# Kernel optimization log

Measured on AMD Instinct MI355X. Metric: run time of the kernel, lower is better.

The kernel has to match this reference:

```python
import jax, jax.numpy as jnp
import numpy as np

V = 32000   # target_vocab_size
E = 512     # embedding_dim
L = 2       # enc_lstm_layers
HD = 512    # enc_lstm_hidden_dim (bidirectional encoder)
H = 2 * HD  # decoder LSTM hidden size
B = 16
T = 128
BOS = 1
CTX = L * 2 * HD          # stepwise context dim = 2048
IN0 = E + CTX             # decoder LSTM layer-0 input dim = 2560


def setup_inputs() -> dict:
    key = jax.random.key(0)
    ks = jax.random.split(key, 12)
    def w(k, shape, fan_in):
        return jax.random.normal(k, shape, jnp.float32) * np.float32(1.0 / np.sqrt(fan_in))
    return {
        "enc_lstm_hidden": jax.random.normal(ks[0], (2 * L, B, HD), jnp.float32),
        "enc_lstm_ctxt": jax.random.normal(ks[1], (2 * L, B, HD), jnp.float32),
        "minibatch_target": jax.random.randint(ks[2], (B, T), 0, V, dtype=jnp.int32),
        "emb": w(ks[3], (V, E), E),
        "w_ih_0": w(ks[4], (4 * H, IN0), IN0),
        "w_hh_0": w(ks[5], (4 * H, H), H),
        "b_ih_0": jnp.zeros((4 * H,), jnp.float32),
        "b_hh_0": jnp.zeros((4 * H,), jnp.float32),
        "w_ih_1": w(ks[6], (4 * H, H), H),
        "w_hh_1": w(ks[7], (4 * H, H), H),
        "b_ih_1": jnp.zeros((4 * H,), jnp.float32),
        "b_hh_1": jnp.zeros((4 * H,), jnp.float32),
        "fc_w": w(ks[8], (V, H), H),
        "fc_b": jnp.zeros((V,), jnp.float32),
    }


def _lstm_layer(x_seq, h0, c0, w_ih, w_hh, b):
    """x_seq: [T, B, in]; returns top outputs [T, B, H]. torch gate order i,f,g,o."""
    def step(carry, x):
        h, c = carry
        g = x @ w_ih.T + h @ w_hh.T + b
        i, f, gg, o = jnp.split(g, 4, axis=-1)
        c = jax.nn.sigmoid(f) * c + jax.nn.sigmoid(i) * jnp.tanh(gg)
        h = jax.nn.sigmoid(o) * jnp.tanh(c)
        return (h, c), h
    (hT, cT), ys = jax.lax.scan(step, (h0, c0), x_seq)
    return ys, hT, cT


def reference(enc_lstm_hidden, enc_lstm_ctxt, minibatch_target, emb,
              w_ih_0, w_hh_0, b_ih_0, b_hh_0,
              w_ih_1, w_hh_1, b_ih_1, b_hh_1, fc_w, fc_b):
    # _reshape_encoder_state: [2L,B,HD] -> [L,B,2HD] (interleave fwd/bwd per layer)
    def reshape_state(s):
        return s.reshape(L, 2, B, HD).transpose(0, 2, 1, 3).reshape(L, B, 2 * HD)
    h0 = reshape_state(enc_lstm_hidden)
    c0 = reshape_state(enc_lstm_ctxt)
    # stepwise input context: [B, 2L*HD]
    ctx = jnp.transpose(enc_lstm_hidden, (1, 0, 2)).reshape(B, CTX)
    # teacher forcing: prev tokens = [BOS, target[:, :-1]]
    tokens = jnp.concatenate(
        [jnp.full((B, 1), BOS, minibatch_target.dtype), minibatch_target[:, :-1]], axis=1)
    tok_emb = emb[tokens]                                   # [B,T,E]
    ctx_b = jnp.broadcast_to(ctx[:, None, :], (B, T, CTX))  # [B,T,CTX]
    x = jnp.concatenate([tok_emb, ctx_b], axis=-1).transpose(1, 0, 2)  # [T,B,IN0]
    x, _, _ = _lstm_layer(x, h0[0], c0[0], w_ih_0, w_hh_0, b_ih_0 + b_hh_0)
    x, _, _ = _lstm_layer(x, h0[1], c0[1], w_ih_1, w_hh_1, b_ih_1 + b_hh_1)
    out = jnp.tanh(x)                                       # [T,B,H]
    logits = jnp.einsum('tbh,vh->btv', out, fc_w) + fc_b    # [B,T,V]
    return logits
```

## Files before the change

kernel.cpp:

```cpp
#include <hip/hip_runtime.h>


#define NBLK 256

typedef float f32x4 __attribute__((ext_vector_type(4)));
typedef __bf16 bf16x8 __attribute__((ext_vector_type(8)));
typedef unsigned short u16;

__device__ __forceinline__ float sigf(float x) { return 1.0f / (1.0f + __expf(-x)); }
__device__ __forceinline__ float tanh_(float x) {
  x = fminf(15.0f, fmaxf(-15.0f, x));
  float e = __expf(2.0f * x);
  return (e - 1.0f) / (e + 1.0f);
}

__device__ __forceinline__ u16 f2bf(float f) {
  __bf16 h = (__bf16)f;
  return __builtin_bit_cast(u16, h);
}

__device__ __forceinline__ void st_cv16(u16* p, u16 v) {
  unsigned vv = v;
  asm volatile("global_store_short %0, %1, off sc0 sc1" :: "v"(p), "v"(vv) : "memory");
}

__device__ __forceinline__ void flag_store(unsigned* p, unsigned v) {
  asm volatile(
      "s_waitcnt vmcnt(0)\n\t"
      "global_store_dword %0, %1, off sc0 sc1"
      :: "v"(p), "v"(v) : "memory");
}

__device__ __forceinline__ void ld4_flags(const unsigned* p, unsigned& a, unsigned& b,
                                          unsigned& c, unsigned& d) {
  asm volatile(
      "global_load_dword %0, %4, off sc0 sc1\n\t"
      "global_load_dword %1, %5, off sc0 sc1\n\t"
      "global_load_dword %2, %6, off sc0 sc1\n\t"
      "global_load_dword %3, %7, off sc0 sc1\n\t"
      "s_waitcnt vmcnt(0)"
      : "=&v"(a), "=&v"(b), "=&v"(c), "=&v"(d)
      : "v"(p), "v"(p + 16), "v"(p + 32), "v"(p + 48)
      : "memory");
}

__device__ __forceinline__ void gsyncf(unsigned step, unsigned* bar) {
  __syncthreads();
  const int tid = threadIdx.x;
  if (tid == 0) flag_store(bar + 16 + blockIdx.x * 16, step);
  if (tid < 64) {
    const unsigned* base = bar + 16 + tid * 64;
    for (;;) {
      unsigned a, b, c, d;
      ld4_flags(base, a, b, c, d);
      bool mine = (a >= step) & (b >= step) & (c >= step) & (d >= step);
      if (__all(mine)) break;
      __builtin_amdgcn_s_sleep(1);
    }
    asm volatile("" ::: "memory");
  }
  __syncthreads();
}

__device__ __forceinline__ void dot4(float& a, float4 wv, float4 xv) {
  a = fmaf(wv.x, xv.x, a);
  a = fmaf(wv.y, xv.y, a);
  a = fmaf(wv.z, xv.z, a);
  a = fmaf(wv.w, xv.w, a);
}

#define MFMA16(ACC, XB, WM, WOFF)                                           \
  _Pragma("unroll")                                                         \
  for (int mm = 0; mm < 16; ++mm) {                                         \
    bf16x8 av = *(const bf16x8*)&XB[fr][mm * 32 + ks8];                     \
    bf16x8 bv = *(const bf16x8*)&WM[fr][(WOFF) + mm * 32 + ks8];            \
    ACC = __builtin_amdgcn_mfma_f32_16x16x32_bf16(av, bv, ACC, 0, 0, 0);    \
  }

__global__ void prep_emb(const int* __restrict__ tgt, const float* __restrict__ emb,
                         u16* __restrict__ x0b) {
  const int g = blockIdx.x * blockDim.x + threadIdx.x;
  const int col8 = (g & 63) * 8;
  const int tb = g >> 6;
  const int t = tb >> 4, b = tb & 15;
  const int tok = (t == 0) ? 1 : tgt[b * 128 + (t - 1)];
  const float* s = emb + (size_t)tok * 512 + col8;
  float4 a = *(const float4*)s;
  float4 bb = *(const float4*)(s + 4);
  __align__(16) u16 r[8] = {f2bf(a.x), f2bf(a.y), f2bf(a.z), f2bf(a.w),
                            f2bf(bb.x), f2bf(bb.y), f2bf(bb.z), f2bf(bb.w)};
  *(uint4*)(x0b + (size_t)tb * 512 + col8) = *(uint4*)r;
}

__global__ __launch_bounds__(256, 1) void prep_ctx(const float* __restrict__ enc_h,
                                                   const float* __restrict__ wih0,
                                                   float* __restrict__ cp) {
  __shared__ float ctx[16][2052];
  const int tid = threadIdx.x;
#pragma unroll
  for (int c = 0; c < 32; ++c) {
    int f4 = tid + c * 256;
    int b = f4 >> 9, kq = f4 & 511;
    *(float4*)&ctx[b][kq * 4] =
        *(const float4*)(enc_h + (kq >> 7) * 8192 + b * 512 + (kq & 127) * 4);
  }
  __syncthreads();
  const int jr = tid >> 4, b = tid & 15;
  const int j = blockIdx.x * 16 + jr;
  const float* w = wih0 + (size_t)j * 2560 + 512;
  float a0 = 0.f, a1 = 0.f, a2 = 0.f, a3 = 0.f;
  for (int k = 0; k < 2048; k += 16) {
    float4 w0 = *(const float4*)(w + k);
    float4 w1 = *(const float4*)(w + k + 4);
    float4 w2 = *(const float4*)(w + k + 8);
    float4 w3 = *(const float4*)(w + k + 12);
    float4 x0 = *(const float4*)&ctx[b][k];
    float4 x1 = *(const float4*)&ctx[b][k + 4];
    float4 x2 = *(const float4*)&ctx[b][k + 8];
    float4 x3 = *(const float4*)&ctx[b][k + 12];
    dot4(a0, w0, x0); dot4(a1, w1, x1); dot4(a2, w2, x2); dot4(a3, w3, x3);
  }
  cp[(size_t)j * 16 + b] = a0 + a1 + a2 + a3;
}

__global__ __launch_bounds__(512, 1) void dec_seq_mf(
    const float* __restrict__ enc_h, const float* __restrict__ enc_c,
    const float* __restrict__ wih0, const float* __restrict__ whh0,
    const float* __restrict__ wih1, const float* __restrict__ whh1,
    const float* __restrict__ bih0, const float* __restrict__ bhh0,
    const float* __restrict__ bih1, const float* __restrict__ bhh1,
    const float* __restrict__ cp, const u16* __restrict__ x0b,
    u16* __restrict__ xr, u16* __restrict__ h1r,
    u16* __restrict__ out2b, unsigned* bar) {
  __shared__ u16 Wa[16][1544];
  __shared__ u16 Wb[16][2056];
  __shared__ u16 xc[2][16][520];
  __shared__ float glsA[16][17];
  __shared__ float glsB[16][17];

  const int tid = threadIdx.x;
  const int wgid = blockIdx.x;
  const int w4 = wgid * 4;
  const int lane = tid & 63;
  const int wave = tid >> 6;
  const int fr = lane & 15;
  const int ks8 = (lane >> 4) * 8;
  unsigned step = 0;

  {
    const int row = tid >> 5;
    const int j = (row >> 2) * 1024 + w4 + (row & 3);
    {
      const int c = (tid & 31) * 16;
      const float* s = wih0 + (size_t)j * 2560 + c;
      __align__(16) u16 r[16];
#pragma unroll
      for (int q = 0; q < 4; ++q) {
        float4 v = *(const float4*)(s + q * 4);
        r[q * 4 + 0] = f2bf(v.x); r[q * 4 + 1] = f2bf(v.y);
        r[q * 4 + 2] = f2bf(v.z); r[q * 4 + 3] = f2bf(v.w);
      }
      *(uint4*)&Wa[row][c] = *(uint4*)&r[0];
      *(uint4*)&Wa[row][c + 8] = *(uint4*)&r[8];
    }
    {
      const int c = (tid & 31) * 32;
      const float* s = whh0 + (size_t)j * 1024 + c;
      __align__(16) u16 r[32];
#pragma unroll
      for (int q = 0; q < 8; ++q) {
        float4 v = *(const float4*)(s + q * 4);
        r[q * 4 + 0] = f2bf(v.x); r[q * 4 + 1] = f2bf(v.y);
        r[q * 4 + 2] = f2bf(v.z); r[q * 4 + 3] = f2bf(v.w);
      }
#pragma unroll
      for (int q = 0; q < 4; ++q) *(uint4*)&Wa[row][512 + c + q * 8] = *(uint4*)&r[q * 8];
    }
    {
      const int c = (tid & 31) * 32;
      const float* s = wih1 + (size_t)j * 1024 + c;
      __align__(16) u16 r[32];
#pragma unroll
      for (int q = 0; q < 8; ++q) {
        float4 v = *(const float4*)(s + q * 4);
        r[q * 4 + 0] = f2bf(v.x); r[q * 4 + 1] = f2bf(v.y);
        r[q * 4 + 2] = f2bf(v.z); r[q * 4 + 3] = f2bf(v.w);
      }
#pragma unroll
      for (int q = 0; q < 4; ++q) *(uint4*)&Wb[row][c + q * 8] = *(uint4*)&r[q * 8];
    }
    {
      const int c = (tid & 31) * 32;
      const float* s = whh1 + (size_t)j * 1024 + c;
      __align__(16) u16 r[32];
#pragma unroll
      for (int q = 0; q < 8; ++q) {
        float4 v = *(const float4*)(s + q * 4);
        r[q * 4 + 0] = f2bf(v.x); r[q * 4 + 1] = f2bf(v.y);
        r[q * 4 + 2] = f2bf(v.z); r[q * 4 + 3] = f2bf(v.w);
      }
#pragma unroll
      for (int q = 0; q < 4; ++q) *(uint4*)&Wb[row][1024 + c + q * 8] = *(uint4*)&r[q * 8];
    }
  }

  const int gdj = tid >> 4;
  const int gb = tid & 15;
  float cpA0 = 0.f, cpA1 = 0.f, cpA2 = 0.f, cpA3 = 0.f;
  float cpB0 = 0.f, cpB1 = 0.f, cpB2 = 0.f, cpB3 = 0.f;
  float c0r = 0.f, c1r = 0.f;
  if (tid < 64) {
    const int jp = w4 + gdj;
    cpA0 = cp[(size_t)(jp) * 16 + gb] + bih0[jp] + bhh0[jp];
    cpA1 = cp[(size_t)(1024 + jp) * 16 + gb] + bih0[1024 + jp] + bhh0[1024 + jp];
    cpA2 = cp[(size_t)(2048 + jp) * 16 + gb] + bih0[2048 + jp] + bhh0[2048 + jp];
    cpA3 = cp[(size_t)(3072 + jp) * 16 + gb] + bih0[3072 + jp] + bhh0[3072 + jp];
    cpB0 = bih1[jp] + bhh1[jp];
    cpB1 = bih1[1024 + jp] + bhh1[1024 + jp];
    cpB2 = bih1[2048 + jp] + bhh1[2048 + jp];
    cpB3 = bih1[3072 + jp] + bhh1[3072 + jp];
    const int dir = jp >> 9, e = jp & 511;
    c0r = enc_c[dir * 8192 + gb * 512 + e];
    c1r = enc_c[(2 + dir) * 8192 + gb * 512 + e];
    st_cv16(xr + gb * 1024 + jp, f2bf(enc_h[dir * 8192 + gb * 512 + e]));
    st_cv16(h1r + gb * 1024 + jp, f2bf(enc_h[(2 + dir) * 8192 + gb * 512 + e]));
  }
  gsyncf(++step, bar);

  const int srow = tid >> 5;
  const int scol = (tid & 31) * 16;

  for (int s = 0; s < 129; ++s) {
    uint4 rA0a = {}, rA0b = {}, rB2a = {}, rB2b = {}, rB3a = {}, rB3b = {};
    uint4 rA1a, rA1b, rA2a, rA2b;
    {
      const u16* slotS = xr + (size_t)s * 16384 + srow * 1024;
      rA1a = *(const uint4*)(slotS + scol);
      rA1b = *(const uint4*)(slotS + scol + 8);
      rA2a = *(const uint4*)(slotS + 512 + scol);
      rA2b = *(const uint4*)(slotS + 512 + scol + 8);
      if (s < 128) {
        const u16* sE = x0b + (size_t)s * 8192 + srow * 512;
        rA0a = *(const uint4*)(sE + scol);
        rA0b = *(const uint4*)(sE + scol + 8);
      }
      if (s >= 1) {
        const u16* sH = h1r + (size_t)(s - 1) * 16384 + srow * 1024;
        rB2a = *(const uint4*)(sH + scol);
        rB2b = *(const uint4*)(sH + scol + 8);
        rB3a = *(const uint4*)(sH + 512 + scol);
        rB3b = *(const uint4*)(sH + 512 + scol + 8);
      }
    }
    f32x4 accA = {0.f, 0.f, 0.f, 0.f}, accB = {0.f, 0.f, 0.f, 0.f};

    if (s < 128) {
      *(uint4*)&xc[0][srow][scol] = rA0a;
      *(uint4*)&xc[0][srow][scol + 8] = rA0b;
    }
    __syncthreads();
    *(uint4*)&xc[1][srow][scol] = rA1a;
    *(uint4*)&xc[1][srow][scol + 8] = rA1b;
    if (wave == 0 && s < 128) { MFMA16(accA, xc[0], Wa, 0) }
    __syncthreads();
    *(uint4*)&xc[0][srow][scol] = rA2a;
    *(uint4*)&xc[0][srow][scol + 8] = rA2b;
    if (wave == 0 && s < 128) { MFMA16(accA, xc[1], Wa, 512) }
    if (wave == 1 && s >= 1) { MFMA16(accB, xc[1], Wb, 0) }
    __syncthreads();
    if (s >= 1) {
      *(uint4*)&xc[1][srow][scol] = rB2a;
      *(uint4*)&xc[1][srow][scol + 8] = rB2b;
    }
    if (wave == 0 && s < 128) { MFMA16(accA, xc[0], Wa, 1024) }
    if (wave == 1 && s >= 1) { MFMA16(accB, xc[0], Wb, 512) }
    __syncthreads();
    if (s >= 1) {
      *(uint4*)&xc[0][srow][scol] = rB3a;
      *(uint4*)&xc[0][srow][scol + 8] = rB3b;
    }
    if (wave == 1 && s >= 1) { MFMA16(accB, xc[1], Wb, 1024) }
    __syncthreads();
    if (wave == 1 && s >= 1) { MFMA16(accB, xc[0], Wb, 1536) }
    if (wave == 0 && s < 128) {
#pragma unroll
      for (int r = 0; r < 4; ++r) glsA[fr][(lane >> 4) * 4 + r] = accA[r];
    }
    if (wave == 1 && s >= 1) {
#pragma unroll
      for (int r = 0; r < 4; ++r) glsB[fr][(lane >> 4) * 4 + r] = accB[r];
    }
    __syncthreads();
    if (tid < 64) {
      const int jp = w4 + gdj;
      if (s < 128) {
        float gi = glsA[gdj][gb] + cpA0;
        float gf = glsA[4 + gdj][gb] + cpA1;
        float gg = glsA[8 + gdj][gb] + cpA2;
        float go = glsA[12 + gdj][gb] + cpA3;
        c0r = sigf(gf) * c0r + sigf(gi) * tanh_(gg);
        float h = sigf(go) * tanh_(c0r);
        st_cv16(xr + (size_t)(s + 1) * 16384 + gb * 1024 + jp, f2bf(h));
      }
      if (s >= 1) {
        float gi = glsB[gdj][gb] + cpB0;
        float gf = glsB[4 + gdj][gb] + cpB1;
        float gg = glsB[8 + gdj][gb] + cpB2;
        float go = glsB[12 + gdj][gb] + cpB3;
        c1r = sigf(gf) * c1r + sigf(gi) * tanh_(gg);
        float h = sigf(go) * tanh_(c1r);
        st_cv16(h1r + (size_t)s * 16384 + gb * 1024 + jp, f2bf(h));
        out2b[((s - 1) * 16 + gb) * 1024 + jp] = f2bf(tanh_(h));
      }
    }
    gsyncf(++step, bar);
  }
}

__global__ __launch_bounds__(256, 2) void fc_gemm_mfma(
    const u16* __restrict__ A, const float* __restrict__ Bw,
    const float* __restrict__ bias, float* __restrict__ C) {
  __shared__ __align__(16) u16 Al[128][40];
  __shared__ __align__(16) u16 Bl[128][40];

  const int tid = threadIdx.x;
  const int m0 = blockIdx.x * 128;
  const int n0 = blockIdx.y * 128;
  const int wave = tid >> 6;
  const int lane = tid & 63;
  const int wm = (wave & 1) * 64;
  const int wn = (wave >> 1) * 64;
  const int fr = lane & 15;
  const int ks = lane >> 4;

  const int srow = tid >> 1;
  const int sh16 = (tid & 1) * 16;

  const u16* Ag = A + (size_t)(m0 + srow) * 1024 + sh16;
  const float* Bg = Bw + (size_t)(n0 + srow) * 1024 + sh16;

  f32x4 acc[4][4] = {};

  for (int k0 = 0; k0 < 1024; k0 += 32) {
    uint4 a0 = *(const uint4*)(Ag + k0);
    uint4 a1 = *(const uint4*)(Ag + k0 + 8);
    float bfv[16];
    *(float4*)&bfv[0] = *(const float4*)(Bg + k0);
    *(float4*)&bfv[4] = *(const float4*)(Bg + k0 + 4);
    *(float4*)&bfv[8] = *(const float4*)(Bg + k0 + 8);
    *(float4*)&bfv[12] = *(const float4*)(Bg + k0 + 12);
    u16 bu[16];
#pragma unroll
    for (int u = 0; u < 16; ++u) bu[u] = f2bf(bfv[u]);

    __syncthreads();
    *(uint4*)&Al[srow][sh16] = a0;
    *(uint4*)&Al[srow][sh16 + 8] = a1;
    *(uint4*)&Bl[srow][sh16] = *(uint4*)&bu[0];
    *(uint4*)&Bl[srow][sh16 + 8] = *(uint4*)&bu[8];
    __syncthreads();

    bf16x8 af[4], bf[4];
#pragma unroll
    for (int i = 0; i < 4; ++i) af[i] = *(const bf16x8*)&Al[wm + i * 16 + fr][ks * 8];
#pragma unroll
    for (int j = 0; j < 4; ++j) bf[j] = *(const bf16x8*)&Bl[wn + j * 16 + fr][ks * 8];
#pragma unroll
    for (int i = 0; i < 4; ++i)
#pragma unroll
      for (int j = 0; j < 4; ++j)
        acc[i][j] = __builtin_amdgcn_mfma_f32_16x16x32_bf16(af[i], bf[j], acc[i][j], 0, 0, 0);
  }

  float bj[4];
#pragma unroll
  for (int j = 0; j < 4; ++j) bj[j] = bias[n0 + wn + j * 16 + fr];

  const int mrb = (lane >> 4) * 4;
#pragma unroll
  for (int i = 0; i < 4; ++i) {
#pragma unroll
    for (int r = 0; r < 4; ++r) {
      const int m = m0 + wm + i * 16 + mrb + r;
      float* dst = C + ((size_t)(m & 15) * 128 + (m >> 4)) * 32000;
#pragma unroll
      for (int j = 0; j < 4; ++j) {
        dst[n0 + wn + j * 16 + fr] = acc[i][j][r] + bj[j];
      }
    }
  }
}

extern "C" void kernel_launch(void* const* d_in, const int* in_sizes, int n_in,
                              void* d_out, int out_size, void* d_ws, size_t ws_size,
                              hipStream_t stream) {
  const float* enc_h = (const float*)d_in[0];
  const float* enc_c = (const float*)d_in[1];
  const int* tgt = (const int*)d_in[2];
  const float* emb = (const float*)d_in[3];
  const float* wih0 = (const float*)d_in[4];
  const float* whh0 = (const float*)d_in[5];
  const float* bih0 = (const float*)d_in[6];
  const float* bhh0 = (const float*)d_in[7];
  const float* wih1 = (const float*)d_in[8];
  const float* whh1 = (const float*)d_in[9];
  const float* bih1 = (const float*)d_in[10];
  const float* bhh1 = (const float*)d_in[11];
  const float* fcw = (const float*)d_in[12];
  const float* fcb = (const float*)d_in[13];
  float* logits = (float*)d_out;

  unsigned* bar = (unsigned*)d_ws;
  hipMemsetAsync(d_ws, 0, 64 + 256 * 64, stream);

  float* cp = (float*)((char*)d_ws + 32768);
  u16* x0b = (u16*)(cp + 65536);
  u16* xr = x0b + 1048576;
  u16* h1r = xr + 2113536;
  u16* out2b = h1r + 2113536;

  prep_emb<<<512, 256, 0, stream>>>(tgt, emb, x0b);
  prep_ctx<<<256, 256, 0, stream>>>(enc_h, wih0, cp);
  dec_seq_mf<<<NBLK, 512, 0, stream>>>(enc_h, enc_c, wih0, whh0, wih1, whh1,
                                       bih0, bhh0, bih1, bhh1, cp, x0b,
                                       xr, h1r, out2b, bar);
  fc_gemm_mfma<<<dim3(16, 250), 256, 0, stream>>>(out2b, fcw, fcb, logits);
}
```

Baseline: 1.098 ms.

## Precompute embedding input projection and split recurrent MFMA work across six waves

The embedding part of the layer-0 input projection is taken out of the sequential loop and computed for all timesteps by a separate bf16 MFMA GEMM (pe_gemm), whose results are added during the gate update. Inside the persistent recurrent kernel, the dot products that used to run serially on waves 0 and 1 are now spread over six waves, one 512-wide K chunk each, with partial sums reduced through shared memory. Each step now needs one barrier to stage inputs instead of several, and one wave keeps part of its weights in registers. The cost is an extra kernel launch, a large fp32 intermediate buffer, and a per-step gather of those values.

```diff
diff --git a/kernel.cpp b/kernel.cpp
--- a/kernel.cpp
+++ b/kernel.cpp
@@ -17,6 +17,13 @@
 __device__ __forceinline__ u16 f2bf(float f) {
   __bf16 h = (__bf16)f;
   return __builtin_bit_cast(u16, h);
+}
+
+__device__ __forceinline__ bf16x8 cvt8(float4 a, float4 b) {
+  bf16x8 v;
+  v[0] = (__bf16)a.x; v[1] = (__bf16)a.y; v[2] = (__bf16)a.z; v[3] = (__bf16)a.w;
+  v[4] = (__bf16)b.x; v[5] = (__bf16)b.y; v[6] = (__bf16)b.z; v[7] = (__bf16)b.w;
+  return v;
 }
 
 __device__ __forceinline__ void st_cv16(u16* p, u16 v) {
@@ -68,14 +75,6 @@
   a = fmaf(wv.z, xv.z, a);
   a = fmaf(wv.w, xv.w, a);
 }
-
-#define MFMA16(ACC, XB, WM, WOFF)                                           \
-  _Pragma("unroll")                                                         \
-  for (int mm = 0; mm < 16; ++mm) {                                         \
-    bf16x8 av = *(const bf16x8*)&XB[fr][mm * 32 + ks8];                     \
-    bf16x8 bv = *(const bf16x8*)&WM[fr][(WOFF) + mm * 32 + ks8];            \
-    ACC = __builtin_amdgcn_mfma_f32_16x16x32_bf16(av, bv, ACC, 0, 0, 0);    \
-  }
 
 __global__ void prep_emb(const int* __restrict__ tgt, const float* __restrict__ emb,
                          u16* __restrict__ x0b) {
@@ -123,84 +122,124 @@
   cp[(size_t)j * 16 + b] = a0 + a1 + a2 + a3;
 }
 
-__global__ __launch_bounds__(512, 1) void dec_seq_mf(
+__global__ __launch_bounds__(256, 2) void pe_gemm(
+    const u16* __restrict__ A, const float* __restrict__ Bw, float* __restrict__ C) {
+  __shared__ __align__(16) u16 Al[128][40];
+  __shared__ __align__(16) u16 Bl[128][40];
+  const int tid = threadIdx.x;
+  const int m0 = blockIdx.x * 128;
+  const int n0 = blockIdx.y * 128;
+  const int wave = tid >> 6;
+  const int lane = tid & 63;
+  const int wm = (wave & 1) * 64;
+  const int wn = (wave >> 1) * 64;
+  const int fr = lane & 15;
+  const int ks = lane >> 4;
+  const int srow = tid >> 1;
+  const int sh16 = (tid & 1) * 16;
+  const u16* Ag = A + (size_t)(m0 + srow) * 512 + sh16;
+  const float* Bg = Bw + (size_t)(n0 + srow) * 2560 + sh16;
+  f32x4 acc[4][4] = {};
+  for (int k0 = 0; k0 < 512; k0 += 32) {
+    uint4 a0 = *(const uint4*)(Ag + k0);
+    uint4 a1 = *(const uint4*)(Ag + k0 + 8);
+    float bfv[16];
+    *(float4*)&bfv[0] = *(const float4*)(Bg + k0);
+    *(float4*)&bfv[4] = *(const float4*)(Bg + k0 + 4);
+    *(float4*)&bfv[8] = *(const float4*)(Bg + k0 + 8);
+    *(float4*)&bfv[12] = *(const float4*)(Bg + k0 + 12);
+    u16 bu[16];
+#pragma unroll
+    for (int u = 0; u < 16; ++u) bu[u] = f2bf(bfv[u]);
+    __syncthreads();
+    *(uint4*)&Al[srow][sh16] = a0;
+    *(uint4*)&Al[srow][sh16 + 8] = a1;
+    *(uint4*)&Bl[srow][sh16] = *(uint4*)&bu[0];
+    *(uint4*)&Bl[srow][sh16 + 8] = *(uint4*)&bu[8];
+    __syncthreads();
+    bf16x8 af[4], bf[4];
+#pragma unroll
+    for (int i = 0; i < 4; ++i) af[i] = *(const bf16x8*)&Al[wm + i * 16 + fr][ks * 8];
+#pragma unroll
+    for (int j = 0; j < 4; ++j) bf[j] = *(const bf16x8*)&Bl[wn + j * 16 + fr][ks * 8];
+#pragma unroll
+    for (int i = 0; i < 4; ++i)
+#pragma unroll
+      for (int j = 0; j < 4; ++j)
+        acc[i][j] = __builtin_amdgcn_mfma_f32_16x16x32_bf16(af[i], bf[j], acc[i][j], 0, 0, 0);
+  }
+  const int mrb = (lane >> 4) * 4;
+#pragma unroll
+  for (int i = 0; i < 4; ++i) {
+#pragma unroll
+    for (int r = 0; r < 4; ++r) {
+      const int m = m0 + wm + i * 16 + mrb + r;
+      float* dst = C + (size_t)m * 4096;
+#pragma unroll
+      for (int j = 0; j < 4; ++j) dst[n0 + wn + j * 16 + fr] = acc[i][j][r];
+    }
+  }
+}
+
+#define BURST_L(ACC, XB, XOFF, WF0)                                        \
+  _Pragma("unroll")                                                        \
+  for (int mm = 0; mm < 16; ++mm) {                                        \
+    bf16x8 av = *(const bf16x8*)&XB[(XOFF) + mm * 520 + lane8];            \
+    bf16x8 bv = *(const bf16x8*)&wf[((WF0) + mm) * 512 + lane8];           \
+    ACC = __builtin_amdgcn_mfma_f32_16x16x32_bf16(av, bv, ACC, 0, 0, 0);   \
+  }
+#define BURST_R(ACC, XB, XOFF)                                             \
+  _Pragma("unroll")                                                        \
+  for (int mm = 0; mm < 16; ++mm) {                                        \
+    bf16x8 av = *(const bf16x8*)&XB[(XOFF) + mm * 520 + lane8];            \
+    ACC = __builtin_amdgcn_mfma_f32_16x16x32_bf16(av, bw[mm], ACC, 0, 0, 0); \
+  }
+
+__global__ __launch_bounds__(512, 1) void dec_seq_mf2(
     const float* __restrict__ enc_h, const float* __restrict__ enc_c,
-    const float* __restrict__ wih0, const float* __restrict__ whh0,
-    const float* __restrict__ wih1, const float* __restrict__ whh1,
+    const float* __restrict__ whh0, const float* __restrict__ wih1,
+    const float* __restrict__ whh1,
     const float* __restrict__ bih0, const float* __restrict__ bhh0,
     const float* __restrict__ bih1, const float* __restrict__ bhh1,
-    const float* __restrict__ cp, const u16* __restrict__ x0b,
+    const float* __restrict__ cp, const float* __restrict__ pe,
     u16* __restrict__ xr, u16* __restrict__ h1r,
     u16* __restrict__ out2b, unsigned* bar) {
-  __shared__ u16 Wa[16][1544];
-  __shared__ u16 Wb[16][2056];
-  __shared__ u16 xc[2][16][520];
-  __shared__ float glsA[16][17];
-  __shared__ float glsB[16][17];
+  __shared__ u16 xf[16640];
+  __shared__ u16 h1f[16640];
+  __shared__ u16 wf[40960];
+  __shared__ float gls[6][16][17];
 
   const int tid = threadIdx.x;
   const int wgid = blockIdx.x;
   const int w4 = wgid * 4;
   const int lane = tid & 63;
   const int wave = tid >> 6;
-  const int fr = lane & 15;
-  const int ks8 = (lane >> 4) * 8;
+  const int lane8 = lane * 8;
   unsigned step = 0;
 
-  {
-    const int row = tid >> 5;
-    const int j = (row >> 2) * 1024 + w4 + (row & 3);
-    {
-      const int c = (tid & 31) * 16;
-      const float* s = wih0 + (size_t)j * 2560 + c;
-      __align__(16) u16 r[16];
-#pragma unroll
-      for (int q = 0; q < 4; ++q) {
-        float4 v = *(const float4*)(s + q * 4);
-        r[q * 4 + 0] = f2bf(v.x); r[q * 4 + 1] = f2bf(v.y);
-        r[q * 4 + 2] = f2bf(v.z); r[q * 4 + 3] = f2bf(v.w);
-      }
-      *(uint4*)&Wa[row][c] = *(uint4*)&r[0];
-      *(uint4*)&Wa[row][c + 8] = *(uint4*)&r[8];
-    }
-    {
-      const int c = (tid & 31) * 32;
-      const float* s = whh0 + (size_t)j * 1024 + c;
-      __align__(16) u16 r[32];
-#pragma unroll
-      for (int q = 0; q < 8; ++q) {
-        float4 v = *(const float4*)(s + q * 4);
-        r[q * 4 + 0] = f2bf(v.x); r[q * 4 + 1] = f2bf(v.y);
-        r[q * 4 + 2] = f2bf(v.z); r[q * 4 + 3] = f2bf(v.w);
-      }
-#pragma unroll
-      for (int q = 0; q < 4; ++q) *(uint4*)&Wa[row][512 + c + q * 8] = *(uint4*)&r[q * 8];
-    }
-    {
-      const int c = (tid & 31) * 32;
-      const float* s = wih1 + (size_t)j * 1024 + c;
-      __align__(16) u16 r[32];
-#pragma unroll
-      for (int q = 0; q < 8; ++q) {
-        float4 v = *(const float4*)(s + q * 4);
-        r[q * 4 + 0] = f2bf(v.x); r[q * 4 + 1] = f2bf(v.y);
-        r[q * 4 + 2] = f2bf(v.z); r[q * 4 + 3] = f2bf(v.w);
-      }
-#pragma unroll
-      for (int q = 0; q < 4; ++q) *(uint4*)&Wb[row][c + q * 8] = *(uint4*)&r[q * 8];
-    }
-    {
-      const int c = (tid & 31) * 32;
-      const float* s = whh1 + (size_t)j * 1024 + c;
-      __align__(16) u16 r[32];
-#pragma unroll
-      for (int q = 0; q < 8; ++q) {
-        float4 v = *(const float4*)(s + q * 4);
-        r[q * 4 + 0] = f2bf(v.x); r[q * 4 + 1] = f2bf(v.y);
-        r[q * 4 + 2] = f2bf(v.z); r[q * 4 + 3] = f2bf(v.w);
-      }
-#pragma unroll
-      for (int q = 0; q < 4; ++q) *(uint4*)&Wb[row][1024 + c + q * 8] = *(uint4*)&r[q * 8];
+  for (int it = 0; it < 10; ++it) {
+    const int slot = tid + it * 512;
+    const int fg = slot >> 6;
+    const int l = slot & 63;
+    const int ch = fg >> 4, mm = fg & 15;
+    const int nn = l & 15;
+    const int j = (nn >> 2) * 1024 + w4 + (nn & 3);
+    const int k = ((ch == 1 || ch == 3) ? 512 : 0) + mm * 32 + ((l >> 4) * 8);
+    const float* src = (ch < 2) ? whh0 : (ch < 4) ? wih1 : whh1;
+    const float* s = src + (size_t)j * 1024 + k;
+    float4 a = *(const float4*)s;
+    float4 b = *(const float4*)(s + 4);
+    bf16x8 v = cvt8(a, b);
+    *(uint4*)&wf[fg * 512 + l * 8] = __builtin_bit_cast(uint4, v);
+  }
+  bf16x8 bw[16];
+  if (wave == 5) {
+    const int nn = lane & 15;
+    const int j = (nn >> 2) * 1024 + w4 + (nn & 3);
+#pragma unroll
+    for (int mm = 0; mm < 16; ++mm) {
+      const float* s = whh1 + (size_t)j * 1024 + 512 + mm * 32 + (lane >> 4) * 8;
+      bw[mm] = cvt8(*(const float4*)s, *(const float4*)(s + 4));
     }
   }
 
@@ -227,86 +266,78 @@
   }
   gsyncf(++step, bar);
 
-  const int srow = tid >> 5;
-  const int scol = (tid & 31) * 16;
+  const int sm = tid >> 5;
+  const int sk0 = (tid & 31) * 8;
 
   for (int s = 0; s < 129; ++s) {
-    uint4 rA0a = {}, rA0b = {}, rB2a = {}, rB2b = {}, rB3a = {}, rB3b = {};
-    uint4 rA1a, rA1b, rA2a, rA2b;
+    const bool doA = (s < 128), doB = (s >= 1);
+    uint4 rx[4], rh[4] = {};
+    float pe0 = 0.f, pe1 = 0.f, pe2 = 0.f, pe3 = 0.f;
     {
-      const u16* slotS = xr + (size_t)s * 16384 + srow * 1024;
-      rA1a = *(const uint4*)(slotS + scol);
-      rA1b = *(const uint4*)(slotS + scol + 8);
-      rA2a = *(const uint4*)(slotS + 512 + scol);
-      rA2b = *(const uint4*)(slotS + 512 + scol + 8);
-      if (s < 128) {
-        const u16* sE = x0b + (size_t)s * 8192 + srow * 512;
-        rA0a = *(const uint4*)(sE + scol);
-        rA0b = *(const uint4*)(sE + scol + 8);
-      }
-      if (s >= 1) {
-        const u16* sH = h1r + (size_t)(s - 1) * 16384 + srow * 1024;
-        rB2a = *(const uint4*)(sH + scol);
-        rB2b = *(const uint4*)(sH + scol + 8);
-        rB3a = *(const uint4*)(sH + 512 + scol);
-        rB3b = *(const uint4*)(sH + 512 + scol + 8);
-      }
-    }
-    f32x4 accA = {0.f, 0.f, 0.f, 0.f}, accB = {0.f, 0.f, 0.f, 0.f};
-
-    if (s < 128) {
-      *(uint4*)&xc[0][srow][scol] = rA0a;
-      *(uint4*)&xc[0][srow][scol + 8] = rA0b;
-    }
-    __syncthreads();
-    *(uint4*)&xc[1][srow][scol] = rA1a;
-    *(uint4*)&xc[1][srow][scol + 8] = rA1b;
-    if (wave == 0 && s < 128) { MFMA16(accA, xc[0], Wa, 0) }
-    __syncthreads();
-    *(uint4*)&xc[0][srow][scol] = rA2a;
-    *(uint4*)&xc[0][srow][scol + 8] = rA2b;
-    if (wave == 0 && s < 128) { MFMA16(accA, xc[1], Wa, 512) }
-    if (wave == 1 && s >= 1) { MFMA16(accB, xc[1], Wb, 0) }
-    __syncthreads();
-    if (s >= 1) {
-      *(uint4*)&xc[1][srow][scol] = rB2a;
-      *(uint4*)&xc[1][srow][scol + 8] = rB2b;
-    }
-    if (wave == 0 && s < 128) { MFMA16(accA, xc[0], Wa, 1024) }
-    if (wave == 1 && s >= 1) { MFMA16(accB, xc[0], Wb, 512) }
-    __syncthreads();
-    if (s >= 1) {
-      *(uint4*)&xc[0][srow][scol] = rB3a;
-      *(uint4*)&xc[0][srow][scol + 8] = rB3b;
-    }
-    if (wave == 1 && s >= 1) { MFMA16(accB, xc[1], Wb, 1024) }
-    __syncthreads();
-    if (wave == 1 && s >= 1) { MFMA16(accB, xc[0], Wb, 1536) }
-    if (wave == 0 && s < 128) {
-#pragma unroll
-      for (int r = 0; r < 4; ++r) glsA[fr][(lane >> 4) * 4 + r] = accA[r];
-    }
-    if (wave == 1 && s >= 1) {
-#pragma unroll
-      for (int r = 0; r < 4; ++r) glsB[fr][(lane >> 4) * 4 + r] = accB[r];
-    }
-    __syncthreads();
+      const u16* sx = xr + (size_t)s * 16384 + sm * 1024;
+#pragma unroll
+      for (int jj = 0; jj < 4; ++jj) rx[jj] = *(const uint4*)(sx + sk0 + jj * 256);
+      if (doB) {
+        const u16* sh = h1r + (size_t)(s - 1) * 16384 + sm * 1024;
+#pragma unroll
+        for (int jj = 0; jj < 4; ++jj) rh[jj] = *(const uint4*)(sh + sk0 + jj * 256);
+      }
+      if (doA && tid < 64) {
+        const float* pp = pe + (size_t)(s * 16 + gb) * 4096 + (w4 + gdj);
+        pe0 = pp[0]; pe1 = pp[1024]; pe2 = pp[2048]; pe3 = pp[3072];
+      }
+    }
+#pragma unroll
+    for (int jj = 0; jj < 4; ++jj) {
+      const int k = sk0 + jj * 256;
+      const int f = k >> 5;
+      const int lt = sm + 16 * ((k >> 3) & 3);
+      *(uint4*)&xf[f * 520 + lt * 8] = rx[jj];
+    }
+    if (doB) {
+#pragma unroll
+      for (int jj = 0; jj < 4; ++jj) {
+        const int k = sk0 + jj * 256;
+        const int f = k >> 5;
+        const int lt = sm + 16 * ((k >> 3) & 3);
+        *(uint4*)&h1f[f * 520 + lt * 8] = rh[jj];
+      }
+    }
+    __syncthreads();
+
+    f32x4 acc = {0.f, 0.f, 0.f, 0.f};
+    if (wave == 0 && doA) { BURST_L(acc, xf, 0, 0) }
+    if (wave == 1 && doA) { BURST_L(acc, xf, 8320, 16) }
+    if (wave == 2 && doB) { BURST_L(acc, xf, 0, 32) }
+    if (wave == 3 && doB) { BURST_L(acc, xf, 8320, 48) }
+    if (wave == 4 && doB) { BURST_L(acc, h1f, 0, 64) }
+    if (wave == 5 && doB) { BURST_R(acc, h1f, 8320) }
+    if ((wave <= 1 && doA) || (wave >= 2 && wave <= 5 && doB)) {
+#pragma unroll
+      for (int r = 0; r < 4; ++r) gls[wave][lane & 15][(lane >> 4) * 4 + r] = acc[r];
+    }
+    __syncthreads();
+
     if (tid < 64) {
       const int jp = w4 + gdj;
-      if (s < 128) {
-        float gi = glsA[gdj][gb] + cpA0;
-        float gf = glsA[4 + gdj][gb] + cpA1;
-        float gg = glsA[8 + gdj][gb] + cpA2;
-        float go = glsA[12 + gdj][gb] + cpA3;
+      if (doA) {
+        float gi = gls[0][gdj][gb] + gls[1][gdj][gb] + pe0 + cpA0;
+        float gf = gls[0][4 + gdj][gb] + gls[1][4 + gdj][gb] + pe1 + cpA1;
+        float gg = gls[0][8 + gdj][gb] + gls[1][8 + gdj][gb] + pe2 + cpA2;
+        float go = gls[0][12 + gdj][gb] + gls[1][12 + gdj][gb] + pe3 + cpA3;
         c0r = sigf(gf) * c0r + sigf(gi) * tanh_(gg);
         float h = sigf(go) * tanh_(c0r);
         st_cv16(xr + (size_t)(s + 1) * 16384 + gb * 1024 + jp, f2bf(h));
       }
-      if (s >= 1) {
-        float gi = glsB[gdj][gb] + cpB0;
-        float gf = glsB[4 + gdj][gb] + cpB1;
-        float gg = glsB[8 + gdj][gb] + cpB2;
-        float go = glsB[12 + gdj][gb] + cpB3;
+      if (doB) {
+        float gi = gls[2][gdj][gb] + gls[3][gdj][gb] + gls[4][gdj][gb] +
+                   gls[5][gdj][gb] + cpB0;
+        float gf = gls[2][4 + gdj][gb] + gls[3][4 + gdj][gb] + gls[4][4 + gdj][gb] +
+                   gls[5][4 + gdj][gb] + cpB1;
+        float gg = gls[2][8 + gdj][gb] + gls[3][8 + gdj][gb] + gls[4][8 + gdj][gb] +
+                   gls[5][8 + gdj][gb] + cpB2;
+        float go = gls[2][12 + gdj][gb] + gls[3][12 + gdj][gb] + gls[4][12 + gdj][gb] +
+                   gls[5][12 + gdj][gb] + cpB3;
         c1r = sigf(gf) * c1r + sigf(gi) * tanh_(gg);
         float h = sigf(go) * tanh_(c1r);
         st_cv16(h1r + (size_t)s * 16384 + gb * 1024 + jp, f2bf(h));
@@ -415,14 +446,16 @@
 
   float* cp = (float*)((char*)d_ws + 32768);
   u16* x0b = (u16*)(cp + 65536);
-  u16* xr = x0b + 1048576;
+  float* pe = (float*)(x0b + 1048576);
+  u16* xr = (u16*)(pe + 8388608);
   u16* h1r = xr + 2113536;
   u16* out2b = h1r + 2113536;
 
   prep_emb<<<512, 256, 0, stream>>>(tgt, emb, x0b);
   prep_ctx<<<256, 256, 0, stream>>>(enc_h, wih0, cp);
-  dec_seq_mf<<<NBLK, 512, 0, stream>>>(enc_h, enc_c, wih0, whh0, wih1, whh1,
-                                       bih0, bhh0, bih1, bhh1, cp, x0b,
-                                       xr, h1r, out2b, bar);
+  pe_gemm<<<dim3(16, 32), 256, 0, stream>>>(x0b, wih0, pe);
+  dec_seq_mf2<<<NBLK, 512, 0, stream>>>(enc_h, enc_c, whh0, wih1, whh1,
+                                        bih0, bhh0, bih1, bhh1, cp, pe,
+                                        xr, h1r, out2b, bar);
   fc_gemm_mfma<<<dim3(16, 250), 256, 0, stream>>>(out2b, fcw, fcb, logits);
 }
```

New measurement: 1.253 ms. 1.14x slower.

## Hold LSTM weights in registers and split K across seven waves

Applied to the files above, without the earlier changes.

Each of seven waves now keeps one 512-wide K-slice of the gate weights in registers (bf16x8 fragments) instead of reading weights from LDS. All activations for the step are staged into LDS at once. The old chain of double-buffered stages and syncs is replaced by a single sync before the MFMA bursts, with partial sums reduced through a shared gate array. This removes the serial MFMA chains on two waves and the weight LDS traffic, so each recurrent step has a shorter critical path. The costs are higher register pressure and a wider reduction in the pointwise stage.

```diff
diff --git a/kernel.cpp b/kernel.cpp
--- a/kernel.cpp
+++ b/kernel.cpp
@@ -17,6 +17,13 @@
 __device__ __forceinline__ u16 f2bf(float f) {
   __bf16 h = (__bf16)f;
   return __builtin_bit_cast(u16, h);
+}
+
+__device__ __forceinline__ bf16x8 cvt8(float4 a, float4 b) {
+  bf16x8 v;
+  v[0] = (__bf16)a.x; v[1] = (__bf16)a.y; v[2] = (__bf16)a.z; v[3] = (__bf16)a.w;
+  v[4] = (__bf16)b.x; v[5] = (__bf16)b.y; v[6] = (__bf16)b.z; v[7] = (__bf16)b.w;
+  return v;
 }
 
 __device__ __forceinline__ void st_cv16(u16* p, u16 v) {
@@ -68,14 +75,6 @@
   a = fmaf(wv.z, xv.z, a);
   a = fmaf(wv.w, xv.w, a);
 }
-
-#define MFMA16(ACC, XB, WM, WOFF)                                           \
-  _Pragma("unroll")                                                         \
-  for (int mm = 0; mm < 16; ++mm) {                                         \
-    bf16x8 av = *(const bf16x8*)&XB[fr][mm * 32 + ks8];                     \
-    bf16x8 bv = *(const bf16x8*)&WM[fr][(WOFF) + mm * 32 + ks8];            \
-    ACC = __builtin_amdgcn_mfma_f32_16x16x32_bf16(av, bv, ACC, 0, 0, 0);    \
-  }
 
 __global__ void prep_emb(const int* __restrict__ tgt, const float* __restrict__ emb,
                          u16* __restrict__ x0b) {
@@ -123,7 +122,14 @@
   cp[(size_t)j * 16 + b] = a0 + a1 + a2 + a3;
 }
 
-__global__ __launch_bounds__(512, 1) void dec_seq_mf(
+#define BURST(ACC, BP, S, XOFF)                                              \
+  _Pragma("unroll")                                                          \
+  for (int mm = 0; mm < 16; ++mm) {                                          \
+    bf16x8 av = *(const bf16x8*)&(BP)[fr * (S) + (XOFF) + mm * 32 + ks8];    \
+    ACC = __builtin_amdgcn_mfma_f32_16x16x32_bf16(av, bw[mm], ACC, 0, 0, 0); \
+  }
+
+__global__ __launch_bounds__(512, 1) void dec_seq_rw(
     const float* __restrict__ enc_h, const float* __restrict__ enc_c,
     const float* __restrict__ wih0, const float* __restrict__ whh0,
     const float* __restrict__ wih1, const float* __restrict__ whh1,
@@ -132,11 +138,10 @@
     const float* __restrict__ cp, const u16* __restrict__ x0b,
     u16* __restrict__ xr, u16* __restrict__ h1r,
     u16* __restrict__ out2b, unsigned* bar) {
-  __shared__ u16 Wa[16][1544];
-  __shared__ u16 Wb[16][2056];
-  __shared__ u16 xc[2][16][520];
-  __shared__ float glsA[16][17];
-  __shared__ float glsB[16][17];
+  __shared__ u16 xe[16 * 520];
+  __shared__ u16 xs[16 * 1032];
+  __shared__ u16 h1s[16 * 1032];
+  __shared__ float gls[7][16][17];
 
   const int tid = threadIdx.x;
   const int wgid = blockIdx.x;
@@ -147,60 +152,30 @@
   const int ks8 = (lane >> 4) * 8;
   unsigned step = 0;
 
+  bf16x8 bw[16];
   {
-    const int row = tid >> 5;
-    const int j = (row >> 2) * 1024 + w4 + (row & 3);
-    {
-      const int c = (tid & 31) * 16;
-      const float* s = wih0 + (size_t)j * 2560 + c;
-      __align__(16) u16 r[16];
-#pragma unroll
-      for (int q = 0; q < 4; ++q) {
-        float4 v = *(const float4*)(s + q * 4);
-        r[q * 4 + 0] = f2bf(v.x); r[q * 4 + 1] = f2bf(v.y);
-        r[q * 4 + 2] = f2bf(v.z); r[q * 4 + 3] = f2bf(v.w);
-      }
-      *(uint4*)&Wa[row][c] = *(uint4*)&r[0];
-      *(uint4*)&Wa[row][c + 8] = *(uint4*)&r[8];
-    }
-    {
-      const int c = (tid & 31) * 32;
-      const float* s = whh0 + (size_t)j * 1024 + c;
-      __align__(16) u16 r[32];
-#pragma unroll
-      for (int q = 0; q < 8; ++q) {
-        float4 v = *(const float4*)(s + q * 4);
-        r[q * 4 + 0] = f2bf(v.x); r[q * 4 + 1] = f2bf(v.y);
-        r[q * 4 + 2] = f2bf(v.z); r[q * 4 + 3] = f2bf(v.w);
-      }
-#pragma unroll
-      for (int q = 0; q < 4; ++q) *(uint4*)&Wa[row][512 + c + q * 8] = *(uint4*)&r[q * 8];
-    }
-    {
-      const int c = (tid & 31) * 32;
-      const float* s = wih1 + (size_t)j * 1024 + c;
-      __align__(16) u16 r[32];
-#pragma unroll
-      for (int q = 0; q < 8; ++q) {
-        float4 v = *(const float4*)(s + q * 4);
-        r[q * 4 + 0] = f2bf(v.x); r[q * 4 + 1] = f2bf(v.y);
-        r[q * 4 + 2] = f2bf(v.z); r[q * 4 + 3] = f2bf(v.w);
-      }
-#pragma unroll
-      for (int q = 0; q < 4; ++q) *(uint4*)&Wb[row][c + q * 8] = *(uint4*)&r[q * 8];
-    }
-    {
-      const int c = (tid & 31) * 32;
-      const float* s = whh1 + (size_t)j * 1024 + c;
-      __align__(16) u16 r[32];
-#pragma unroll
-      for (int q = 0; q < 8; ++q) {
-        float4 v = *(const float4*)(s + q * 4);
-        r[q * 4 + 0] = f2bf(v.x); r[q * 4 + 1] = f2bf(v.y);
-        r[q * 4 + 2] = f2bf(v.z); r[q * 4 + 3] = f2bf(v.w);
-      }
-#pragma unroll
-      for (int q = 0; q < 4; ++q) *(uint4*)&Wb[row][1024 + c + q * 8] = *(uint4*)&r[q * 8];
+    const int nn = lane & 15;
+    const int j = (nn >> 2) * 1024 + w4 + (nn & 3);
+    const float* wsrc = nullptr;
+    size_t wstride = 1024;
+    int wko = 0;
+    if (wave == 0) { wsrc = wih0; wstride = 2560; wko = 0; }
+    else if (wave == 1) { wsrc = whh0; wko = 0; }
+    else if (wave == 2) { wsrc = whh0; wko = 512; }
+    else if (wave == 3) { wsrc = wih1; wko = 0; }
+    else if (wave == 4) { wsrc = wih1; wko = 512; }
+    else if (wave == 5) { wsrc = whh1; wko = 0; }
+    else if (wave == 6) { wsrc = whh1; wko = 512; }
+    if (wsrc) {
+      const float* base = wsrc + (size_t)j * wstride + wko + (lane >> 4) * 8;
+#pragma unroll
+      for (int mm = 0; mm < 16; ++mm) {
+        const float* sp = base + mm * 32;
+        bw[mm] = cvt8(*(const float4*)sp, *(const float4*)(sp + 4));
+      }
+    } else {
+#pragma unroll
+      for (int mm = 0; mm < 16; ++mm) bw[mm] = bf16x8{};
     }
   }
 
@@ -227,86 +202,75 @@
   }
   gsyncf(++step, bar);
 
-  const int srow = tid >> 5;
-  const int scol = (tid & 31) * 16;
+  const int sm = tid >> 5;
+  const int skq = (tid & 31) * 8;
 
   for (int s = 0; s < 129; ++s) {
-    uint4 rA0a = {}, rA0b = {}, rB2a = {}, rB2b = {}, rB3a = {}, rB3b = {};
-    uint4 rA1a, rA1b, rA2a, rA2b;
+    const bool doA = (s < 128), doB = (s >= 1);
+
+    uint4 rx[4], rh[4] = {}, re[2] = {};
     {
-      const u16* slotS = xr + (size_t)s * 16384 + srow * 1024;
-      rA1a = *(const uint4*)(slotS + scol);
-      rA1b = *(const uint4*)(slotS + scol + 8);
-      rA2a = *(const uint4*)(slotS + 512 + scol);
-      rA2b = *(const uint4*)(slotS + 512 + scol + 8);
-      if (s < 128) {
-        const u16* sE = x0b + (size_t)s * 8192 + srow * 512;
-        rA0a = *(const uint4*)(sE + scol);
-        rA0b = *(const uint4*)(sE + scol + 8);
-      }
-      if (s >= 1) {
-        const u16* sH = h1r + (size_t)(s - 1) * 16384 + srow * 1024;
-        rB2a = *(const uint4*)(sH + scol);
-        rB2b = *(const uint4*)(sH + scol + 8);
-        rB3a = *(const uint4*)(sH + 512 + scol);
-        rB3b = *(const uint4*)(sH + 512 + scol + 8);
-      }
-    }
-    f32x4 accA = {0.f, 0.f, 0.f, 0.f}, accB = {0.f, 0.f, 0.f, 0.f};
-
-    if (s < 128) {
-      *(uint4*)&xc[0][srow][scol] = rA0a;
-      *(uint4*)&xc[0][srow][scol + 8] = rA0b;
+      const u16* sx = xr + (size_t)s * 16384 + sm * 1024;
+#pragma unroll
+      for (int jj = 0; jj < 4; ++jj) rx[jj] = *(const uint4*)(sx + skq + jj * 256);
+      if (doB) {
+        const u16* sh = h1r + (size_t)(s - 1) * 16384 + sm * 1024;
+#pragma unroll
+        for (int jj = 0; jj < 4; ++jj) rh[jj] = *(const uint4*)(sh + skq + jj * 256);
+      }
+      if (doA) {
+        const u16* se = x0b + (size_t)s * 8192 + sm * 512;
+#pragma unroll
+        for (int jj = 0; jj < 2; ++jj) re[jj] = *(const uint4*)(se + skq + jj * 256);
+      }
+    }
+#pragma unroll
+    for (int jj = 0; jj < 4; ++jj) *(uint4*)&xs[sm * 1032 + skq + jj * 256] = rx[jj];
+    if (doB) {
+#pragma unroll
+      for (int jj = 0; jj < 4; ++jj) *(uint4*)&h1s[sm * 1032 + skq + jj * 256] = rh[jj];
+    }
+    if (doA) {
+#pragma unroll
+      for (int jj = 0; jj < 2; ++jj) *(uint4*)&xe[sm * 520 + skq + jj * 256] = re[jj];
     }
     __syncthreads();
-    *(uint4*)&xc[1][srow][scol] = rA1a;
-    *(uint4*)&xc[1][srow][scol + 8] = rA1b;
-    if (wave == 0 && s < 128) { MFMA16(accA, xc[0], Wa, 0) }
+
+    f32x4 acc = {0.f, 0.f, 0.f, 0.f};
+    bool act = false;
+    if (wave == 0) { if (doA) { BURST(acc, xe, 520, 0) act = true; } }
+    else if (wave == 1) { if (doA) { BURST(acc, xs, 1032, 0) act = true; } }
+    else if (wave == 2) { if (doA) { BURST(acc, xs, 1032, 512) act = true; } }
+    else if (wave == 3) { if (doB) { BURST(acc, xs, 1032, 0) act = true; } }
+    else if (wave == 4) { if (doB) { BURST(acc, xs, 1032, 512) act = true; } }
+    else if (wave == 5) { if (doB) { BURST(acc, h1s, 1032, 0) act = true; } }
+    else if (wave == 6) { if (doB) { BURST(acc, h1s, 1032, 512) act = true; } }
+    if (act) {
+#pragma unroll
+      for (int r = 0; r < 4; ++r) gls[wave][fr][(lane >> 4) * 4 + r] = acc[r];
+    }
     __syncthreads();
-    *(uint4*)&xc[0][srow][scol] = rA2a;
-    *(uint4*)&xc[0][srow][scol + 8] = rA2b;
-    if (wave == 0 && s < 128) { MFMA16(accA, xc[1], Wa, 512) }
-    if (wave == 1 && s >= 1) { MFMA16(accB, xc[1], Wb, 0) }
-    __syncthreads();
-    if (s >= 1) {
-      *(uint4*)&xc[1][srow][scol] = rB2a;
-      *(uint4*)&xc[1][srow][scol + 8] = rB2b;
-    }
-    if (wave == 0 && s < 128) { MFMA16(accA, xc[0], Wa, 1024) }
-    if (wave == 1 && s >= 1) { MFMA16(accB, xc[0], Wb, 512) }
-    __syncthreads();
-    if (s >= 1) {
-      *(uint4*)&xc[0][srow][scol] = rB3a;
-      *(uint4*)&xc[0][srow][scol + 8] = rB3b;
-    }
-    if (wave == 1 && s >= 1) { MFMA16(accB, xc[1], Wb, 1024) }
-    __syncthreads();
-    if (wave == 1 && s >= 1) { MFMA16(accB, xc[0], Wb, 1536) }
-    if (wave == 0 && s < 128) {
-#pragma unroll
-      for (int r = 0; r < 4; ++r) glsA[fr][(lane >> 4) * 4 + r] = accA[r];
-    }
-    if (wave == 1 && s >= 1) {
-#pragma unroll
-      for (int r = 0; r < 4; ++r) glsB[fr][(lane >> 4) * 4 + r] = accB[r];
-    }
-    __syncthreads();
+
     if (tid < 64) {
       const int jp = w4 + gdj;
-      if (s < 128) {
-        float gi = glsA[gdj][gb] + cpA0;
-        float gf = glsA[4 + gdj][gb] + cpA1;
-        float gg = glsA[8 + gdj][gb] + cpA2;
-        float go = glsA[12 + gdj][gb] + cpA3;
+      if (doA) {
+        float gi = gls[0][gdj][gb] + gls[1][gdj][gb] + gls[2][gdj][gb] + cpA0;
+        float gf = gls[0][4 + gdj][gb] + gls[1][4 + gdj][gb] + gls[2][4 + gdj][gb] + cpA1;
+        float gg = gls[0][8 + gdj][gb] + gls[1][8 + gdj][gb] + gls[2][8 + gdj][gb] + cpA2;
+        float go = gls[0][12 + gdj][gb] + gls[1][12 + gdj][gb] + gls[2][12 + gdj][gb] + cpA3;
         c0r = sigf(gf) * c0r + sigf(gi) * tanh_(gg);
         float h = sigf(go) * tanh_(c0r);
         st_cv16(xr + (size_t)(s + 1) * 16384 + gb * 1024 + jp, f2bf(h));
       }
-      if (s >= 1) {
-        float gi = glsB[gdj][gb] + cpB0;
-        float gf = glsB[4 + gdj][gb] + cpB1;
-        float gg = glsB[8 + gdj][gb] + cpB2;
-        float go = glsB[12 + gdj][gb] + cpB3;
+      if (doB) {
+        float gi = gls[3][gdj][gb] + gls[4][gdj][gb] + gls[5][gdj][gb] +
+                   gls[6][gdj][gb] + cpB0;
+        float gf = gls[3][4 + gdj][gb] + gls[4][4 + gdj][gb] + gls[5][4 + gdj][gb] +
+                   gls[6][4 + gdj][gb] + cpB1;
+        float gg = gls[3][8 + gdj][gb] + gls[4][8 + gdj][gb] + gls[5][8 + gdj][gb] +
+                   gls[6][8 + gdj][gb] + cpB2;
+        float go = gls[3][12 + gdj][gb] + gls[4][12 + gdj][gb] + gls[5][12 + gdj][gb] +
+                   gls[6][12 + gdj][gb] + cpB3;
         c1r = sigf(gf) * c1r + sigf(gi) * tanh_(gg);
         float h = sigf(go) * tanh_(c1r);
         st_cv16(h1r + (size_t)s * 16384 + gb * 1024 + jp, f2bf(h));
@@ -421,7 +385,7 @@
 
   prep_emb<<<512, 256, 0, stream>>>(tgt, emb, x0b);
   prep_ctx<<<256, 256, 0, stream>>>(enc_h, wih0, cp);
-  dec_seq_mf<<<NBLK, 512, 0, stream>>>(enc_h, enc_c, wih0, whh0, wih1, whh1,
+  dec_seq_rw<<<NBLK, 512, 0, stream>>>(enc_h, enc_c, wih0, whh0, wih1, whh1,
                                        bih0, bhh0, bih1, bhh1, cp, x0b,
                                        xr, h1r, out2b, bar);
   fc_gemm_mfma<<<dim3(16, 250), 256, 0, stream>>>(out2b, fcw, fcb, logits);
```

Measured after the change: 1.081 ms. About the same (-1.6%).
